# Performance work log

Hardware: AMD Instinct MI355X
Metric: run time of the kernel (lower is better)

The kernel has to match this reference:

```python
import jax, jax.numpy as jnp
import numpy as np

HEAD_NUM = 8
HEAD_DIM = 32
EPS = 0.0  # torch.linalg.norm division has no eps; keep exact


def setup_inputs() -> dict:
    key = jax.random.key(0)
    k1, k2 = jax.random.split(key)
    batch_s = jax.random.normal(k1, (2048, HEAD_NUM * HEAD_DIM), dtype=jnp.float32)
    batch_ro = jax.random.normal(k2, (8192, HEAD_NUM * HEAD_DIM), dtype=jnp.float32)
    return {"batch_s": batch_s, "batch_ro": batch_ro}


def reference(batch_s, batch_ro):
    N, M = batch_s.shape[0], batch_ro.shape[0]
    s = batch_s.reshape(N, HEAD_NUM, HEAD_DIM)   # [N, H, D]
    ro = batch_ro.reshape(M, HEAD_NUM, HEAD_DIM)  # [M, H, D]
    # L2-normalize each head vector
    s = s / jnp.linalg.norm(s, axis=-1, keepdims=True)
    ro = ro / jnp.linalg.norm(ro, axis=-1, keepdims=True)
    # per-head cosine similarity: [N, M, H]
    dist = jnp.einsum('nhd,mhd->nmh', s, ro)
    # max-pool over heads -> [N, M]
    return jnp.max(dist, axis=-1)
```

## Files before the change

kernel.cpp:

```cpp
#include <hip/hip_runtime.h>

#define S_ROWS 2048
#define RO_ROWS 8192
#define HEADS 8
#define HDIM 32
#define ROWLEN 256

typedef __attribute__((ext_vector_type(8))) short bf16x8;
typedef __attribute__((ext_vector_type(4))) float f32x4;
typedef __attribute__((ext_vector_type(4))) short s16x4;

__device__ __forceinline__ short f32_to_bf16_rne(float f) {
    union { float f; unsigned u; } v; v.f = f;
    return (short)((v.u + 0x7fffu + ((v.u >> 16) & 1u)) >> 16);
}

__global__ __launch_bounds__(256) void mhd_normalize(const float* __restrict__ s,
                                                     const float* __restrict__ ro,
                                                     short* __restrict__ outN) {
    const int idx = blockIdx.x * 256 + threadIdx.x;
    const int S_TOT4 = S_ROWS * ROWLEN / 4;
    f32x4 x = (idx < S_TOT4) ? ((const f32x4*)s)[idx]
                             : ((const f32x4*)ro)[idx - S_TOT4];
    float ss = x[0] * x[0] + x[1] * x[1] + x[2] * x[2] + x[3] * x[3];
    ss += __shfl_xor(ss, 1);
    ss += __shfl_xor(ss, 2);
    ss += __shfl_xor(ss, 4);
    const float inv = rsqrtf(ss);
    s16x4 r;
    r[0] = f32_to_bf16_rne(x[0] * inv);
    r[1] = f32_to_bf16_rne(x[1] * inv);
    r[2] = f32_to_bf16_rne(x[2] * inv);
    r[3] = f32_to_bf16_rne(x[3] * inv);
    ((s16x4*)outN)[idx] = r;
}

__global__ __launch_bounds__(256) void mhd_dist(const short* __restrict__ sN,
                                                const short* __restrict__ roN,
                                                float* __restrict__ out) {
    const int lane = threadIdx.x & 63;
    const int wave = threadIdx.x >> 6;
    const int wr = wave >> 1;
    const int wc = wave & 1;
    const int tile_r = blockIdx.x >> 6;
    const int tile_c = blockIdx.x & 63;
    const int row0 = tile_r * 128 + wr * 64;
    const int col0 = tile_c * 128 + wc * 64;
    const int l15 = lane & 15;
    const int kg = lane >> 4;

    f32x4 runmax[4][4];
#pragma unroll
    for (int i = 0; i < 4; ++i)
#pragma unroll
        for (int j = 0; j < 4; ++j)
            runmax[i][j] = (f32x4){-3.0e38f, -3.0e38f, -3.0e38f, -3.0e38f};

    const size_t aBase = (size_t)(row0 + l15) * ROWLEN + kg * 8;
    const size_t bBase = (size_t)(col0 + l15) * ROWLEN + kg * 8;

#pragma unroll 1
    for (int h = 0; h < HEADS; ++h) {
        const size_t hoff = (size_t)h * HDIM;
        bf16x8 a[4], b[4];
#pragma unroll
        for (int i = 0; i < 4; ++i) {
            a[i] = *(const bf16x8*)(sN + aBase + (size_t)i * 16 * ROWLEN + hoff);
            b[i] = *(const bf16x8*)(roN + bBase + (size_t)i * 16 * ROWLEN + hoff);
        }
#pragma unroll
        for (int i = 0; i < 4; ++i)
#pragma unroll
            for (int j = 0; j < 4; ++j) {
                f32x4 acc = {0.f, 0.f, 0.f, 0.f};
                acc = __builtin_amdgcn_mfma_f32_16x16x32_bf16(b[j], a[i], acc, 0, 0, 0);
#pragma unroll
                for (int q = 0; q < 4; ++q)
                    runmax[i][j][q] = fmaxf(runmax[i][j][q], acc[q]);
            }
    }

#pragma unroll
    for (int i = 0; i < 4; ++i) {
        float* rowp = out + (size_t)(row0 + i * 16 + l15) * RO_ROWS + col0 + kg * 4;
#pragma unroll
        for (int j = 0; j < 4; ++j)
            *(f32x4*)(rowp + j * 16) = runmax[i][j];
    }
}

extern "C" void kernel_launch(void* const* d_in, const int* in_sizes, int n_in,
                              void* d_out, int out_size, void* d_ws, size_t ws_size,
                              hipStream_t stream) {
    const float* batch_s  = (const float*)d_in[0];
    const float* batch_ro = (const float*)d_in[1];
    float* out = (float*)d_out;

    short* sN  = (short*)d_ws;
    short* roN = sN + (size_t)S_ROWS * ROWLEN;

    const int totalV4 = (S_ROWS + RO_ROWS) * ROWLEN / 4;
    mhd_normalize<<<totalV4 / 256, 256, 0, stream>>>(batch_s, batch_ro, sN);

    mhd_dist<<<(S_ROWS / 128) * (RO_ROWS / 128), 256, 0, stream>>>(sN, roN, out);
}
```

Measured before the change: 113.3 us.

## Pre-tile normalized inputs per head and stage output through LDS for coalesced stores

```diff
diff --git a/kernel.cpp b/kernel.cpp
--- a/kernel.cpp
+++ b/kernel.cpp
@@ -5,6 +5,8 @@
 #define HEADS 8
 #define HDIM 32
 #define ROWLEN 256
+#define NB_S (S_ROWS / 16)
+#define NB_RO (RO_ROWS / 16)
 
 typedef __attribute__((ext_vector_type(8))) short bf16x8;
 typedef __attribute__((ext_vector_type(4))) float f32x4;
@@ -17,11 +19,13 @@
 
 __global__ __launch_bounds__(256) void mhd_normalize(const float* __restrict__ s,
                                                      const float* __restrict__ ro,
-                                                     short* __restrict__ outN) {
+                                                     short* __restrict__ sF,
+                                                     short* __restrict__ roF) {
     const int idx = blockIdx.x * 256 + threadIdx.x;
     const int S_TOT4 = S_ROWS * ROWLEN / 4;
-    f32x4 x = (idx < S_TOT4) ? ((const f32x4*)s)[idx]
-                             : ((const f32x4*)ro)[idx - S_TOT4];
+    const bool isS = idx < S_TOT4;
+    const int li = isS ? idx : idx - S_TOT4;
+    f32x4 x = isS ? ((const f32x4*)s)[li] : ((const f32x4*)ro)[li];
     float ss = x[0] * x[0] + x[1] * x[1] + x[2] * x[2] + x[3] * x[3];
     ss += __shfl_xor(ss, 1);
     ss += __shfl_xor(ss, 2);
@@ -32,20 +36,27 @@
     r[1] = f32_to_bf16_rne(x[1] * inv);
     r[2] = f32_to_bf16_rne(x[2] * inv);
     r[3] = f32_to_bf16_rne(x[3] * inv);
-    ((s16x4*)outN)[idx] = r;
+
+    const int n   = li >> 6;
+    const int rem = li & 63;
+    const int h   = rem >> 3;
+    const int dg  = rem & 7;
+    const int NB  = isS ? NB_S : NB_RO;
+    short* base   = isS ? sF : roF;
+    const size_t off = (((size_t)(h * NB + (n >> 4)) * 16 + (n & 15)) * 32) + dg * 4;
+    *(s16x4*)(base + off) = r;
 }
 
-__global__ __launch_bounds__(256) void mhd_dist(const short* __restrict__ sN,
-                                                const short* __restrict__ roN,
-                                                float* __restrict__ out) {
+__global__ __launch_bounds__(256, 4) void mhd_dist(const short* __restrict__ sF,
+                                                   const short* __restrict__ roF,
+                                                   float* __restrict__ out) {
+    __shared__ float lds[4][16][68];
     const int lane = threadIdx.x & 63;
     const int wave = threadIdx.x >> 6;
     const int wr = wave >> 1;
     const int wc = wave & 1;
     const int tile_r = blockIdx.x >> 6;
     const int tile_c = blockIdx.x & 63;
-    const int row0 = tile_r * 128 + wr * 64;
-    const int col0 = tile_c * 128 + wc * 64;
     const int l15 = lane & 15;
     const int kg = lane >> 4;
 
@@ -56,17 +67,19 @@
         for (int j = 0; j < 4; ++j)
             runmax[i][j] = (f32x4){-3.0e38f, -3.0e38f, -3.0e38f, -3.0e38f};
 
-    const size_t aBase = (size_t)(row0 + l15) * ROWLEN + kg * 8;
-    const size_t bBase = (size_t)(col0 + l15) * ROWLEN + kg * 8;
+    const int nbA = tile_r * 8 + wr * 4;
+    const int nbB = tile_c * 8 + wc * 4;
+    const size_t laneOff = (size_t)l15 * 32 + kg * 8;
 
 #pragma unroll 1
     for (int h = 0; h < HEADS; ++h) {
-        const size_t hoff = (size_t)h * HDIM;
+        const short* aBase = sF  + (size_t)(h * NB_S  + nbA) * 512 + laneOff;
+        const short* bBase = roF + (size_t)(h * NB_RO + nbB) * 512 + laneOff;
         bf16x8 a[4], b[4];
 #pragma unroll
         for (int i = 0; i < 4; ++i) {
-            a[i] = *(const bf16x8*)(sN + aBase + (size_t)i * 16 * ROWLEN + hoff);
-            b[i] = *(const bf16x8*)(roN + bBase + (size_t)i * 16 * ROWLEN + hoff);
+            a[i] = *(const bf16x8*)(aBase + (size_t)i * 512);
+            b[i] = *(const bf16x8*)(bBase + (size_t)i * 512);
         }
 #pragma unroll
         for (int i = 0; i < 4; ++i)
@@ -80,12 +93,21 @@
             }
     }
 
+    float* outBase = out + (size_t)(tile_r * 128 + wr * 64) * RO_ROWS
+                         + tile_c * 128 + wc * 64;
+    const int srow = lane >> 4;
+    const int scol = (lane & 15) * 4;
 #pragma unroll
     for (int i = 0; i < 4; ++i) {
-        float* rowp = out + (size_t)(row0 + i * 16 + l15) * RO_ROWS + col0 + kg * 4;
 #pragma unroll
         for (int j = 0; j < 4; ++j)
-            *(f32x4*)(rowp + j * 16) = runmax[i][j];
+            *(f32x4*)&lds[wave][l15][kg * 4 + j * 16] = runmax[i][j];
+#pragma unroll
+        for (int t = 0; t < 4; ++t) {
+            const int rowL = t * 4 + srow;
+            f32x4 v = *(const f32x4*)&lds[wave][rowL][scol];
+            *(f32x4*)(outBase + (size_t)(i * 16 + rowL) * RO_ROWS + scol) = v;
+        }
     }
 }
 
@@ -96,11 +118,11 @@
     const float* batch_ro = (const float*)d_in[1];
     float* out = (float*)d_out;
 
-    short* sN  = (short*)d_ws;
-    short* roN = sN + (size_t)S_ROWS * ROWLEN;
+    short* sF  = (short*)d_ws;
+    short* roF = sF + (size_t)S_ROWS * ROWLEN;
 
     const int totalV4 = (S_ROWS + RO_ROWS) * ROWLEN / 4;
-    mhd_normalize<<<totalV4 / 256, 256, 0, stream>>>(batch_s, batch_ro, sN);
+    mhd_normalize<<<totalV4 / 256, 256, 0, stream>>>(batch_s, batch_ro, sF, roF);
 
-    mhd_dist<<<(S_ROWS / 128) * (RO_ROWS / 128), 256, 0, stream>>>(sN, roN, out);
+    mhd_dist<<<(S_ROWS / 128) * (RO_ROWS / 128), 256, 0, stream>>>(sF, roF, out);
 }
```

Measured after the change: 97.35 us. 1.16x faster.
